# Optimization experiments

Hardware: AMD Instinct MI355X
Metric: run time of the kernel (lower is better)

The kernel has to match this reference:

```python
import jax, jax.numpy as jnp
import numpy as np

SEQ_LEN = 4096
DIM_HALF = 2048  # x last dim = 2 * DIM_HALF
DIM_OUT = 1024
LN_EPS = 1e-5


def setup_inputs() -> dict:
    key = jax.random.key(0)
    k1, k2, k3 = jax.random.split(key, 3)
    x = jax.random.normal(k1, (SEQ_LEN, 2 * DIM_HALF), dtype=jnp.float32)
    ln_scale = jnp.ones((DIM_HALF,), dtype=jnp.float32)
    # original init is uniform(-eps/n, eps/n); scale randn similarly small
    spatial_weights = jax.random.normal(k2, (SEQ_LEN, SEQ_LEN), dtype=jnp.float32) * (0.001 / SEQ_LEN)
    spatial_biases = jnp.ones((SEQ_LEN, 1), dtype=jnp.float32)
    proj_w = jax.random.normal(k3, (DIM_HALF, DIM_OUT), dtype=jnp.float32) * (1.0 / np.sqrt(DIM_HALF))
    proj_b = jnp.zeros((DIM_OUT,), dtype=jnp.float32)
    return {"x": x, "ln_scale": ln_scale, "spatial_weights": spatial_weights,
            "spatial_biases": spatial_biases, "proj_w": proj_w, "proj_b": proj_b}


def reference(x, ln_scale, spatial_weights, spatial_biases, proj_w, proj_b):
    # split into value half and gate half
    xh, gate = jnp.split(x, 2, axis=-1)  # each (n, d)
    # LayerNorm (scale only, no offset), haiku default eps=1e-5
    mean = jnp.mean(gate, axis=-1, keepdims=True)
    var = jnp.var(gate, axis=-1, keepdims=True)
    gate = (gate - mean) * jax.lax.rsqrt(var + LN_EPS) * ln_scale
    # causal (lower-triangular) masked spatial mixing: out[m,d] = sum_n w[m,n] * gate[n,d]
    n = spatial_weights.shape[0]
    w = jnp.tril(spatial_weights)
    gate = jnp.einsum('nd,mn->md', gate, w) + spatial_biases  # (n, d)
    # gating multiply + output projection
    out = (xh * gate) @ proj_w + proj_b  # (n, dim_out)
    return out
```

## Files before the change

kernel.cpp:

```cpp
#include <hip/hip_runtime.h>
#include <cstdint>
#include <cstddef>
#include <math.h>

#define SEQ 4096
#define DH 2048
#define DOUT 1024

typedef float f32x4 __attribute__((ext_vector_type(4)));
typedef __bf16 bf16x8 __attribute__((ext_vector_type(8)));


__device__ __forceinline__ unsigned short f2bf(float f) {
  unsigned int u = __float_as_uint(f);
  unsigned int r = (u + 0x7FFFu + ((u >> 16) & 1u)) >> 16;
  return (unsigned short)r;
}

__device__ __forceinline__ void g2l16(const unsigned short* g, unsigned short* l) {
  __builtin_amdgcn_global_load_lds((__attribute__((address_space(1))) void*)(void*)g,
                                   (__attribute__((address_space(3))) void*)l, 16, 0, 0);
}


__global__ __launch_bounds__(256) void ln_stats(const float* __restrict__ x,
                                                float* __restrict__ mv,
                                                float* __restrict__ rv) {
  int row = blockIdx.x;
  const float4* g4 = (const float4*)(x + (size_t)row * (2 * DH) + DH);
  float4 a = g4[threadIdx.x];
  float4 b = g4[threadIdx.x + 256];
  float s  = a.x + a.y + a.z + a.w + b.x + b.y + b.z + b.w;
  float s2 = a.x * a.x + a.y * a.y + a.z * a.z + a.w * a.w +
             b.x * b.x + b.y * b.y + b.z * b.z + b.w * b.w;
#pragma unroll
  for (int o = 32; o > 0; o >>= 1) {
    s  += __shfl_down(s, o);
    s2 += __shfl_down(s2, o);
  }
  __shared__ float red[8];
  int wave = threadIdx.x >> 6;
  if ((threadIdx.x & 63) == 0) { red[wave] = s; red[wave + 4] = s2; }
  __syncthreads();
  if (threadIdx.x == 0) {
    float S  = red[0] + red[1] + red[2] + red[3];
    float S2 = red[4] + red[5] + red[6] + red[7];
    float mean = S * (1.0f / DH);
    float var  = S2 * (1.0f / DH) - mean * mean;
    mv[row] = mean;
    rv[row] = rsqrtf(var + 1e-5f);
  }
}


__global__ __launch_bounds__(256) void norm_tr(const float* __restrict__ x,
                                               const float* __restrict__ mv,
                                               const float* __restrict__ rv,
                                               const float* __restrict__ lns,
                                               unsigned short* __restrict__ gateT) {
  __shared__ float tile[64][65];
  int d0 = blockIdx.x * 64;
  int n0 = blockIdx.y * 64;
#pragma unroll
  for (int i = 0; i < 16; i++) {
    int idx = threadIdx.x + i * 256;
    int r = idx >> 6, c = idx & 63;
    float v = x[(size_t)(n0 + r) * (2 * DH) + DH + d0 + c];
    tile[r][c] = (v - mv[n0 + r]) * rv[n0 + r];
  }
  __syncthreads();
#pragma unroll
  for (int i = 0; i < 16; i++) {
    int idx = threadIdx.x + i * 256;
    int dr = idx >> 6, nc = idx & 63;
    float v = tile[nc][dr] * lns[d0 + dr];
    gateT[(size_t)(d0 + dr) * SEQ + n0 + nc] = f2bf(v);
  }
}


__global__ __launch_bounds__(256) void cast_w_tril(const float* __restrict__ w,
                                                   unsigned short* __restrict__ wb) {
  int t = blockIdx.x;
  int i0 = (int)((sqrtf(8.f * (float)t + 1.f) - 1.f) * 0.5f);
  while ((i0 + 1) * (i0 + 2) / 2 <= t) i0++;
  while (i0 * (i0 + 1) / 2 > t) i0--;
  int j0 = t - i0 * (i0 + 1) / 2;
  const bool interior = (j0 < i0);
  const int rowBase = i0 * 128, colBase = j0 * 128;
#pragma unroll
  for (int rnd = 0; rnd < 8; rnd++) {
    int idx = rnd * 256 + threadIdx.x;
    int r = idx >> 4, g = idx & 15;
    int m = rowBase + r, k = colBase + g * 8;
    size_t e = (size_t)m * SEQ + k;
    uint4 o;
    if (interior || k + 7 <= m) {
      const float4* s = (const float4*)(w + e);
      float4 a = s[0], b = s[1];
      o.x = (unsigned)f2bf(a.x) | ((unsigned)f2bf(a.y) << 16);
      o.y = (unsigned)f2bf(a.z) | ((unsigned)f2bf(a.w) << 16);
      o.z = (unsigned)f2bf(b.x) | ((unsigned)f2bf(b.y) << 16);
      o.w = (unsigned)f2bf(b.z) | ((unsigned)f2bf(b.w) << 16);
    } else if (k > m) {
      o.x = o.y = o.z = o.w = 0u;
    } else {
      unsigned short tt[8];
#pragma unroll
      for (int j = 0; j < 8; j++) tt[j] = (k + j <= m) ? f2bf(w[e + j]) : (unsigned short)0;
      o.x = (unsigned)tt[0] | ((unsigned)tt[1] << 16);
      o.y = (unsigned)tt[2] | ((unsigned)tt[3] << 16);
      o.z = (unsigned)tt[4] | ((unsigned)tt[5] << 16);
      o.w = (unsigned)tt[6] | ((unsigned)tt[7] << 16);
    }
    *(uint4*)(wb + e) = o;
  }
}


__global__ __launch_bounds__(256) void proj_tr(const float* __restrict__ pw,
                                               unsigned short* __restrict__ pT) {
  __shared__ float tile[64][65];
  int j0 = blockIdx.x * 64;
  int d0 = blockIdx.y * 64;
#pragma unroll
  for (int i = 0; i < 16; i++) {
    int idx = threadIdx.x + i * 256;
    int r = idx >> 6, c = idx & 63;
    tile[r][c] = pw[(size_t)(d0 + r) * DOUT + j0 + c];
  }
  __syncthreads();
#pragma unroll
  for (int i = 0; i < 16; i++) {
    int idx = threadIdx.x + i * 256;
    int jr = idx >> 6, dc = idx & 63;
    pT[(size_t)(j0 + jr) * DH + d0 + dc] = f2bf(tile[dc][jr]);
  }
}


template <bool PAIR, int EPI>
__global__ __launch_bounds__(256) void gemm_db(const unsigned short* __restrict__ A,
                                               const unsigned short* __restrict__ BT,
                                               const float* __restrict__ xfull,
                                               const float* __restrict__ rbias,
                                               unsigned short* __restrict__ Pout,
                                               const float* __restrict__ cbias,
                                               float* __restrict__ out,
                                               int N, int K) {
  constexpr int BK = 64;
  __shared__ unsigned short sA0[128 * BK];
  __shared__ unsigned short sA1[128 * BK];
  __shared__ unsigned short sB0[64 * BK];
  __shared__ unsigned short sB1[64 * BK];

  const int tid = threadIdx.x;
  const int lane = tid & 63, wave = tid >> 6;
  const int quad = lane >> 4, l16 = lane & 15;
  const int wm = wave >> 1, wn = wave & 1;
  const int bn0 = blockIdx.x * 64;
  const int p = blockIdx.y;

  const int bm0a = p * 128;
  const int bm0b = PAIR ? (2 * (int)gridDim.y - 1 - p) * 128 : 0;
  const int e1 = PAIR ? 2 * (p + 1) : 0x7fffffff;
  const int total = PAIR ? (2 + 4 * (int)gridDim.y) : (K / BK);

  int sOff[4], sDst[4];
#pragma unroll
  for (int r = 0; r < 4; r++) {
    int idx = r * 256 + tid;
    int row = idx >> 3;
    sOff[r] = row * K + (((idx & 7) ^ (row & 7)) * 8);
    sDst[r] = idx * 8;
  }

  f32x4 acc[4][2] = {};

  auto stage = [&](int i, unsigned short* dA, unsigned short* dB) {
    int kk, bm;
    if (!PAIR || i < e1) { kk = i * BK; bm = bm0a; }
    else                 { kk = (i - e1) * BK; bm = bm0b; }
    const unsigned short* Ab = A + (size_t)bm * K + kk;
    const unsigned short* Bb = BT + (size_t)bn0 * K + kk;
#pragma unroll
    for (int r = 0; r < 4; r++) g2l16(Ab + sOff[r], dA + sDst[r]);
#pragma unroll
    for (int r = 0; r < 2; r++) g2l16(Bb + sOff[r], dB + sDst[r]);
  };

  auto compute = [&](const unsigned short* cA, const unsigned short* cB) {
    bf16x8 af[2][4], bf[2][2];
#pragma unroll
    for (int h = 0; h < 2; h++) {
#pragma unroll
      for (int i = 0; i < 4; i++) {
        int R = wm * 64 + i * 16 + l16;
        af[h][i] = *(const bf16x8*)&cA[R * BK + (((h * 4 + quad) ^ (R & 7)) * 8)];
      }
#pragma unroll
      for (int j = 0; j < 2; j++) {
        int R = wn * 32 + j * 16 + l16;
        bf[h][j] = *(const bf16x8*)&cB[R * BK + (((h * 4 + quad) ^ (R & 7)) * 8)];
      }
    }
#pragma unroll
    for (int h = 0; h < 2; h++)
#pragma unroll
      for (int i = 0; i < 4; i++)
#pragma unroll
        for (int j = 0; j < 2; j++)
          acc[i][j] = __builtin_amdgcn_mfma_f32_16x16x32_bf16(af[h][i], bf[h][j], acc[i][j], 0, 0, 0);
  };

  auto epilogue = [&](int bm0) {
#pragma unroll
    for (int i = 0; i < 4; i++) {
#pragma unroll
      for (int j = 0; j < 2; j++) {
        int col = bn0 + wn * 32 + j * 16 + l16;
#pragma unroll
        for (int r = 0; r < 4; r++) {
          int row = bm0 + wm * 64 + i * 16 + quad * 4 + r;
          float v = acc[i][j][r];
          if (EPI == 1) {
            float g = v + rbias[row];
            float pv = xfull[(size_t)row * (2 * DH) + col] * g;
            Pout[(size_t)row * N + col] = f2bf(pv);
          } else {
            out[(size_t)row * N + col] = v + cbias[col];
          }
        }
      }
    }
  };

  stage(0, sA0, sB0);
  __syncthreads();
  for (int i = 0; i < total; i += 2) {
    stage(i + 1, sA1, sB1);
    compute(sA0, sB0);
    __syncthreads();
    if (i + 2 < total) stage(i + 2, sA0, sB0);
    compute(sA1, sB1);
    if (PAIR && (i + 1) == e1 - 1) {
      epilogue(bm0a);
#pragma unroll
      for (int a = 0; a < 4; a++)
#pragma unroll
        for (int b = 0; b < 2; b++) acc[a][b] = (f32x4){0.f, 0.f, 0.f, 0.f};
    }
    __syncthreads();
  }
  epilogue(PAIR ? bm0b : bm0a);
}


extern "C" void kernel_launch(void* const* d_in, const int* in_sizes, int n_in,
                              void* d_out, int out_size, void* d_ws, size_t ws_size,
                              hipStream_t stream) {
  (void)in_sizes; (void)n_in; (void)out_size; (void)ws_size;
  const float* x   = (const float*)d_in[0];
  const float* lns = (const float*)d_in[1];
  const float* w   = (const float*)d_in[2];
  const float* sb  = (const float*)d_in[3];
  const float* pw  = (const float*)d_in[4];
  const float* pb  = (const float*)d_in[5];
  float* out = (float*)d_out;

  char* p = (char*)d_ws;
  unsigned short* gateT = (unsigned short*)p; p += (size_t)DH * SEQ * 2;
  unsigned short* wb    = (unsigned short*)p; p += (size_t)SEQ * SEQ * 2;
  unsigned short* projT = (unsigned short*)p; p += (size_t)DOUT * DH * 2;
  unsigned short* Pbuf  = (unsigned short*)p; p += (size_t)SEQ * DH * 2;
  float* mv = (float*)p; p += (size_t)SEQ * 4;
  float* rv = (float*)p; p += (size_t)SEQ * 4;

  ln_stats<<<SEQ, 256, 0, stream>>>(x, mv, rv);
  norm_tr<<<dim3(DH / 64, SEQ / 64), 256, 0, stream>>>(x, mv, rv, lns, gateT);
  cast_w_tril<<<528, 256, 0, stream>>>(w, wb);
  proj_tr<<<dim3(DOUT / 64, DH / 64), 256, 0, stream>>>(pw, projT);

  gemm_db<true, 1><<<dim3(DH / 64, SEQ / 256), 256, 0, stream>>>(
      wb, gateT, x, sb, Pbuf, nullptr, nullptr, DH, SEQ);
  gemm_db<false, 2><<<dim3(DOUT / 64, SEQ / 128), 256, 0, stream>>>(
      Pbuf, projT, nullptr, nullptr, nullptr, pb, out, DOUT, DH);
}
```

Baseline: 262.9 us.

## Fuse prep kernels into one launch and enlarge GEMM tiles to 128x128

The four preprocessing kernels (LayerNorm stats, normalize+transpose, masked weight cast, projection transpose) are merged into one launch that dispatches on block index. Row statistics now stay in shared memory, so the stats buffer and its round trip are gone. Both GEMMs move from 128x64 to 128x128 tiles to raise data reuse per block. The causal GEMM drops its paired-row-block load balancing for a simple remapped row order. This risks imbalance across blocks. The LayerNorm part now runs on only 64 blocks that each loop over 32 tiles, which may create a long serial tail.

```diff
diff --git a/kernel.cpp b/kernel.cpp
--- a/kernel.cpp
+++ b/kernel.cpp
@@ -23,148 +23,142 @@
 }
 
 
-__global__ __launch_bounds__(256) void ln_stats(const float* __restrict__ x,
-                                                float* __restrict__ mv,
-                                                float* __restrict__ rv) {
-  int row = blockIdx.x;
-  const float4* g4 = (const float4*)(x + (size_t)row * (2 * DH) + DH);
-  float4 a = g4[threadIdx.x];
-  float4 b = g4[threadIdx.x + 256];
-  float s  = a.x + a.y + a.z + a.w + b.x + b.y + b.z + b.w;
-  float s2 = a.x * a.x + a.y * a.y + a.z * a.z + a.w * a.w +
-             b.x * b.x + b.y * b.y + b.z * b.z + b.w * b.w;
-#pragma unroll
-  for (int o = 32; o > 0; o >>= 1) {
-    s  += __shfl_down(s, o);
-    s2 += __shfl_down(s2, o);
-  }
-  __shared__ float red[8];
-  int wave = threadIdx.x >> 6;
-  if ((threadIdx.x & 63) == 0) { red[wave] = s; red[wave + 4] = s2; }
-  __syncthreads();
-  if (threadIdx.x == 0) {
-    float S  = red[0] + red[1] + red[2] + red[3];
-    float S2 = red[4] + red[5] + red[6] + red[7];
-    float mean = S * (1.0f / DH);
-    float var  = S2 * (1.0f / DH) - mean * mean;
-    mv[row] = mean;
-    rv[row] = rsqrtf(var + 1e-5f);
-  }
-}
-
-
-__global__ __launch_bounds__(256) void norm_tr(const float* __restrict__ x,
-                                               const float* __restrict__ mv,
-                                               const float* __restrict__ rv,
-                                               const float* __restrict__ lns,
-                                               unsigned short* __restrict__ gateT) {
+__global__ __launch_bounds__(256) void prep_fused(const float* __restrict__ x,
+                                                  const float* __restrict__ lns,
+                                                  const float* __restrict__ w,
+                                                  const float* __restrict__ pw,
+                                                  unsigned short* __restrict__ gateT,
+                                                  unsigned short* __restrict__ wb,
+                                                  unsigned short* __restrict__ pT) {
   __shared__ float tile[64][65];
-  int d0 = blockIdx.x * 64;
-  int n0 = blockIdx.y * 64;
-#pragma unroll
-  for (int i = 0; i < 16; i++) {
-    int idx = threadIdx.x + i * 256;
-    int r = idx >> 6, c = idx & 63;
-    float v = x[(size_t)(n0 + r) * (2 * DH) + DH + d0 + c];
-    tile[r][c] = (v - mv[n0 + r]) * rv[n0 + r];
-  }
-  __syncthreads();
-#pragma unroll
-  for (int i = 0; i < 16; i++) {
-    int idx = threadIdx.x + i * 256;
-    int dr = idx >> 6, nc = idx & 63;
-    float v = tile[nc][dr] * lns[d0 + dr];
-    gateT[(size_t)(d0 + dr) * SEQ + n0 + nc] = f2bf(v);
-  }
-}
-
-
-__global__ __launch_bounds__(256) void cast_w_tril(const float* __restrict__ w,
-                                                   unsigned short* __restrict__ wb) {
-  int t = blockIdx.x;
-  int i0 = (int)((sqrtf(8.f * (float)t + 1.f) - 1.f) * 0.5f);
-  while ((i0 + 1) * (i0 + 2) / 2 <= t) i0++;
-  while (i0 * (i0 + 1) / 2 > t) i0--;
-  int j0 = t - i0 * (i0 + 1) / 2;
-  const bool interior = (j0 < i0);
-  const int rowBase = i0 * 128, colBase = j0 * 128;
-#pragma unroll
-  for (int rnd = 0; rnd < 8; rnd++) {
-    int idx = rnd * 256 + threadIdx.x;
-    int r = idx >> 4, g = idx & 15;
-    int m = rowBase + r, k = colBase + g * 8;
-    size_t e = (size_t)m * SEQ + k;
-    uint4 o;
-    if (interior || k + 7 <= m) {
-      const float4* s = (const float4*)(w + e);
-      float4 a = s[0], b = s[1];
-      o.x = (unsigned)f2bf(a.x) | ((unsigned)f2bf(a.y) << 16);
-      o.y = (unsigned)f2bf(a.z) | ((unsigned)f2bf(a.w) << 16);
-      o.z = (unsigned)f2bf(b.x) | ((unsigned)f2bf(b.y) << 16);
-      o.w = (unsigned)f2bf(b.z) | ((unsigned)f2bf(b.w) << 16);
-    } else if (k > m) {
-      o.x = o.y = o.z = o.w = 0u;
-    } else {
-      unsigned short tt[8];
-#pragma unroll
-      for (int j = 0; j < 8; j++) tt[j] = (k + j <= m) ? f2bf(w[e + j]) : (unsigned short)0;
-      o.x = (unsigned)tt[0] | ((unsigned)tt[1] << 16);
-      o.y = (unsigned)tt[2] | ((unsigned)tt[3] << 16);
-      o.z = (unsigned)tt[4] | ((unsigned)tt[5] << 16);
-      o.w = (unsigned)tt[6] | ((unsigned)tt[7] << 16);
-    }
-    *(uint4*)(wb + e) = o;
-  }
-}
-
-
-__global__ __launch_bounds__(256) void proj_tr(const float* __restrict__ pw,
-                                               unsigned short* __restrict__ pT) {
-  __shared__ float tile[64][65];
-  int j0 = blockIdx.x * 64;
-  int d0 = blockIdx.y * 64;
-#pragma unroll
-  for (int i = 0; i < 16; i++) {
-    int idx = threadIdx.x + i * 256;
-    int r = idx >> 6, c = idx & 63;
-    tile[r][c] = pw[(size_t)(d0 + r) * DOUT + j0 + c];
-  }
-  __syncthreads();
-#pragma unroll
-  for (int i = 0; i < 16; i++) {
-    int idx = threadIdx.x + i * 256;
-    int jr = idx >> 6, dc = idx & 63;
-    pT[(size_t)(j0 + jr) * DH + d0 + dc] = f2bf(tile[dc][jr]);
-  }
-}
-
-
-template <bool PAIR, int EPI>
-__global__ __launch_bounds__(256) void gemm_db(const unsigned short* __restrict__ A,
-                                               const unsigned short* __restrict__ BT,
-                                               const float* __restrict__ xfull,
-                                               const float* __restrict__ rbias,
-                                               unsigned short* __restrict__ Pout,
-                                               const float* __restrict__ cbias,
-                                               float* __restrict__ out,
-                                               int N, int K) {
+  __shared__ float smv[64], srv[64];
+  const int tid = threadIdx.x;
+  const int bid = blockIdx.x;
+
+  if (bid < 64) {
+    const int n0 = bid * 64;
+    const int wv = tid >> 6, lane = tid & 63;
+    for (int i = 0; i < 16; i++) {
+      int r = wv * 16 + i;
+      const float4* base = (const float4*)(x + (size_t)(n0 + r) * (2 * DH) + DH);
+      float s = 0.f, s2 = 0.f;
+#pragma unroll
+      for (int it = 0; it < 8; it++) {
+        float4 v = base[lane + it * 64];
+        s  += v.x + v.y + v.z + v.w;
+        s2 += v.x * v.x + v.y * v.y + v.z * v.z + v.w * v.w;
+      }
+#pragma unroll
+      for (int o = 32; o > 0; o >>= 1) {
+        s  += __shfl_down(s, o);
+        s2 += __shfl_down(s2, o);
+      }
+      if (lane == 0) {
+        float mean = s * (1.0f / DH);
+        float var  = s2 * (1.0f / DH) - mean * mean;
+        smv[r] = mean;
+        srv[r] = rsqrtf(var + 1e-5f);
+      }
+    }
+    __syncthreads();
+    for (int dt = 0; dt < 32; dt++) {
+      int d0 = dt * 64;
+#pragma unroll
+      for (int i = 0; i < 16; i++) {
+        int idx = tid + i * 256;
+        int r = idx >> 6, c = idx & 63;
+        float v = x[(size_t)(n0 + r) * (2 * DH) + DH + d0 + c];
+        tile[r][c] = (v - smv[r]) * srv[r];
+      }
+      __syncthreads();
+#pragma unroll
+      for (int i = 0; i < 16; i++) {
+        int idx = tid + i * 256;
+        int dr = idx >> 6, nc = idx & 63;
+        gateT[(size_t)(d0 + dr) * SEQ + n0 + nc] = f2bf(tile[nc][dr] * lns[d0 + dr]);
+      }
+      __syncthreads();
+    }
+  } else if (bid < 592) {
+    int t = bid - 64;
+    int i0 = (int)((sqrtf(8.f * (float)t + 1.f) - 1.f) * 0.5f);
+    while ((i0 + 1) * (i0 + 2) / 2 <= t) i0++;
+    while (i0 * (i0 + 1) / 2 > t) i0--;
+    int j0 = t - i0 * (i0 + 1) / 2;
+    const bool interior = (j0 < i0);
+    const int rowBase = i0 * 128, colBase = j0 * 128;
+#pragma unroll
+    for (int rnd = 0; rnd < 8; rnd++) {
+      int idx = rnd * 256 + tid;
+      int r = idx >> 4, g = idx & 15;
+      int m = rowBase + r, k = colBase + g * 8;
+      size_t e = (size_t)m * SEQ + k;
+      uint4 o;
+      if (interior || k + 7 <= m) {
+        const float4* s = (const float4*)(w + e);
+        float4 a = s[0], b = s[1];
+        o.x = (unsigned)f2bf(a.x) | ((unsigned)f2bf(a.y) << 16);
+        o.y = (unsigned)f2bf(a.z) | ((unsigned)f2bf(a.w) << 16);
+        o.z = (unsigned)f2bf(b.x) | ((unsigned)f2bf(b.y) << 16);
+        o.w = (unsigned)f2bf(b.z) | ((unsigned)f2bf(b.w) << 16);
+      } else if (k > m) {
+        o.x = o.y = o.z = o.w = 0u;
+      } else {
+        unsigned short tt[8];
+#pragma unroll
+        for (int j = 0; j < 8; j++) tt[j] = (k + j <= m) ? f2bf(w[e + j]) : (unsigned short)0;
+        o.x = (unsigned)tt[0] | ((unsigned)tt[1] << 16);
+        o.y = (unsigned)tt[2] | ((unsigned)tt[3] << 16);
+        o.z = (unsigned)tt[4] | ((unsigned)tt[5] << 16);
+        o.w = (unsigned)tt[6] | ((unsigned)tt[7] << 16);
+      }
+      *(uint4*)(wb + e) = o;
+    }
+  } else {
+    int t = bid - 592;
+    int j0 = (t & 15) * 64, d0 = (t >> 4) * 64;
+#pragma unroll
+    for (int i = 0; i < 16; i++) {
+      int idx = tid + i * 256;
+      int r = idx >> 6, c = idx & 63;
+      tile[r][c] = pw[(size_t)(d0 + r) * DOUT + j0 + c];
+    }
+    __syncthreads();
+#pragma unroll
+    for (int i = 0; i < 16; i++) {
+      int idx = tid + i * 256;
+      int jr = idx >> 6, dc = idx & 63;
+      pT[(size_t)(j0 + jr) * DH + d0 + dc] = f2bf(tile[dc][jr]);
+    }
+  }
+}
+
+
+template <bool CAUSAL, int EPI>
+__global__ __launch_bounds__(256) void gemm128db(const unsigned short* __restrict__ A,
+                                                 const unsigned short* __restrict__ BT,
+                                                 const float* __restrict__ xfull,
+                                                 const float* __restrict__ rbias,
+                                                 unsigned short* __restrict__ Pout,
+                                                 const float* __restrict__ cbias,
+                                                 float* __restrict__ out,
+                                                 int N, int K) {
   constexpr int BK = 64;
   __shared__ unsigned short sA0[128 * BK];
   __shared__ unsigned short sA1[128 * BK];
-  __shared__ unsigned short sB0[64 * BK];
-  __shared__ unsigned short sB1[64 * BK];
+  __shared__ unsigned short sB0[128 * BK];
+  __shared__ unsigned short sB1[128 * BK];
 
   const int tid = threadIdx.x;
   const int lane = tid & 63, wave = tid >> 6;
   const int quad = lane >> 4, l16 = lane & 15;
   const int wm = wave >> 1, wn = wave & 1;
-  const int bn0 = blockIdx.x * 64;
-  const int p = blockIdx.y;
-
-  const int bm0a = p * 128;
-  const int bm0b = PAIR ? (2 * (int)gridDim.y - 1 - p) * 128 : 0;
-  const int e1 = PAIR ? 2 * (p + 1) : 0x7fffffff;
-  const int total = PAIR ? (2 + 4 * (int)gridDim.y) : (K / BK);
+  const int bn0 = blockIdx.x * 128;
+
+  int by = blockIdx.y;
+  if (CAUSAL) by = (by < 16) ? by : 47 - by;
+  const int bm0 = by * 128;
+  const int kIters = CAUSAL ? 2 * (by + 1) : (K / BK);
 
   int sOff[4], sDst[4];
 #pragma unroll
@@ -174,23 +168,21 @@
     sOff[r] = row * K + (((idx & 7) ^ (row & 7)) * 8);
     sDst[r] = idx * 8;
   }
-
-  f32x4 acc[4][2] = {};
+  const unsigned short* Ab = A + (size_t)bm0 * K;
+  const unsigned short* Bb = BT + (size_t)bn0 * K;
+
+  f32x4 acc[4][4] = {};
 
   auto stage = [&](int i, unsigned short* dA, unsigned short* dB) {
-    int kk, bm;
-    if (!PAIR || i < e1) { kk = i * BK; bm = bm0a; }
-    else                 { kk = (i - e1) * BK; bm = bm0b; }
-    const unsigned short* Ab = A + (size_t)bm * K + kk;
-    const unsigned short* Bb = BT + (size_t)bn0 * K + kk;
-#pragma unroll
-    for (int r = 0; r < 4; r++) g2l16(Ab + sOff[r], dA + sDst[r]);
-#pragma unroll
-    for (int r = 0; r < 2; r++) g2l16(Bb + sOff[r], dB + sDst[r]);
+    int kk = i * BK;
+#pragma unroll
+    for (int r = 0; r < 4; r++) g2l16(Ab + kk + sOff[r], dA + sDst[r]);
+#pragma unroll
+    for (int r = 0; r < 4; r++) g2l16(Bb + kk + sOff[r], dB + sDst[r]);
   };
 
   auto compute = [&](const unsigned short* cA, const unsigned short* cB) {
-    bf16x8 af[2][4], bf[2][2];
+    bf16x8 af[2][4], bf[2][4];
 #pragma unroll
     for (int h = 0; h < 2; h++) {
 #pragma unroll
@@ -199,8 +191,8 @@
         af[h][i] = *(const bf16x8*)&cA[R * BK + (((h * 4 + quad) ^ (R & 7)) * 8)];
       }
 #pragma unroll
-      for (int j = 0; j < 2; j++) {
-        int R = wn * 32 + j * 16 + l16;
+      for (int j = 0; j < 4; j++) {
+        int R = wn * 64 + j * 16 + l16;
         bf[h][j] = *(const bf16x8*)&cB[R * BK + (((h * 4 + quad) ^ (R & 7)) * 8)];
       }
     }
@@ -209,50 +201,40 @@
 #pragma unroll
       for (int i = 0; i < 4; i++)
 #pragma unroll
-        for (int j = 0; j < 2; j++)
+        for (int j = 0; j < 4; j++)
           acc[i][j] = __builtin_amdgcn_mfma_f32_16x16x32_bf16(af[h][i], bf[h][j], acc[i][j], 0, 0, 0);
   };
 
-  auto epilogue = [&](int bm0) {
-#pragma unroll
-    for (int i = 0; i < 4; i++) {
-#pragma unroll
-      for (int j = 0; j < 2; j++) {
-        int col = bn0 + wn * 32 + j * 16 + l16;
-#pragma unroll
-        for (int r = 0; r < 4; r++) {
-          int row = bm0 + wm * 64 + i * 16 + quad * 4 + r;
-          float v = acc[i][j][r];
-          if (EPI == 1) {
-            float g = v + rbias[row];
-            float pv = xfull[(size_t)row * (2 * DH) + col] * g;
-            Pout[(size_t)row * N + col] = f2bf(pv);
-          } else {
-            out[(size_t)row * N + col] = v + cbias[col];
-          }
-        }
-      }
-    }
-  };
-
   stage(0, sA0, sB0);
   __syncthreads();
-  for (int i = 0; i < total; i += 2) {
+  for (int i = 0; i < kIters; i += 2) {
     stage(i + 1, sA1, sB1);
     compute(sA0, sB0);
     __syncthreads();
-    if (i + 2 < total) stage(i + 2, sA0, sB0);
+    if (i + 2 < kIters) stage(i + 2, sA0, sB0);
     compute(sA1, sB1);
-    if (PAIR && (i + 1) == e1 - 1) {
-      epilogue(bm0a);
-#pragma unroll
-      for (int a = 0; a < 4; a++)
-#pragma unroll
-        for (int b = 0; b < 2; b++) acc[a][b] = (f32x4){0.f, 0.f, 0.f, 0.f};
-    }
-    __syncthreads();
-  }
-  epilogue(PAIR ? bm0b : bm0a);
+    __syncthreads();
+  }
+
+#pragma unroll
+  for (int i = 0; i < 4; i++) {
+#pragma unroll
+    for (int j = 0; j < 4; j++) {
+      int col = bn0 + wn * 64 + j * 16 + l16;
+#pragma unroll
+      for (int r = 0; r < 4; r++) {
+        int row = bm0 + wm * 64 + i * 16 + quad * 4 + r;
+        float v = acc[i][j][r];
+        if (EPI == 1) {
+          float g = v + rbias[row];
+          float pv = xfull[(size_t)row * (2 * DH) + col] * g;
+          Pout[(size_t)row * N + col] = f2bf(pv);
+        } else {
+          out[(size_t)row * N + col] = v + cbias[col];
+        }
+      }
+    }
+  }
 }
 
 
@@ -273,16 +255,11 @@
   unsigned short* wb    = (unsigned short*)p; p += (size_t)SEQ * SEQ * 2;
   unsigned short* projT = (unsigned short*)p; p += (size_t)DOUT * DH * 2;
   unsigned short* Pbuf  = (unsigned short*)p; p += (size_t)SEQ * DH * 2;
-  float* mv = (float*)p; p += (size_t)SEQ * 4;
-  float* rv = (float*)p; p += (size_t)SEQ * 4;
-
-  ln_stats<<<SEQ, 256, 0, stream>>>(x, mv, rv);
-  norm_tr<<<dim3(DH / 64, SEQ / 64), 256, 0, stream>>>(x, mv, rv, lns, gateT);
-  cast_w_tril<<<528, 256, 0, stream>>>(w, wb);
-  proj_tr<<<dim3(DOUT / 64, DH / 64), 256, 0, stream>>>(pw, projT);
-
-  gemm_db<true, 1><<<dim3(DH / 64, SEQ / 256), 256, 0, stream>>>(
+
+  prep_fused<<<1104, 256, 0, stream>>>(x, lns, w, pw, gateT, wb, projT);
+
+  gemm128db<true, 1><<<dim3(DH / 128, SEQ / 128), 256, 0, stream>>>(
       wb, gateT, x, sb, Pbuf, nullptr, nullptr, DH, SEQ);
-  gemm_db<false, 2><<<dim3(DOUT / 64, SEQ / 128), 256, 0, stream>>>(
+  gemm128db<false, 2><<<dim3(DOUT / 128, SEQ / 128), 256, 0, stream>>>(
       Pbuf, projT, nullptr, nullptr, nullptr, pb, out, DOUT, DH);
 }
```

Result: slower. 477.0 us (+81.4%).
